# Kernel optimization log

Hardware: AMD Instinct MI355X
Metric: run time of the kernel (lower is better)

The kernel has to match this reference:

```python
import jax, jax.numpy as jnp
import numpy as np

B, N, M, D = 1, 16384, 16384, 3
CHUNK = 2048          # x tile size for the online-min KNN pass
NN_WEIGHT = 1.0       # self.nn_weight
# both_ways=False, free_weight=0, ch_normals_K=0 -> only cham_x branch is active


def setup_inputs() -> dict:
    key = jax.random.key(0)
    k1, k2, k3 = jax.random.split(key, 3)
    # LiDAR-like point clouds, scaled to a ~20 m scene extent
    pc1 = jax.random.normal(k1, (B, N, D), dtype=jnp.float32) * 10.0
    est_flow = jax.random.normal(k2, (B, N, D), dtype=jnp.float32) * 0.1
    pc2 = jax.random.normal(k3, (B, M, D), dtype=jnp.float32) * 10.0
    return {"pc1": pc1, "est_flow": est_flow, "pc2": pc2}


def _knn1_l1_dists(x, y):
    """Per-point min L1 distance from x [N,3] to y [M,3], tiled over x.

    Equivalent to knn_points(x, y, K=1, norm=1).dists[..., 0] without
    materializing the full [N, M] distance matrix.
    """
    n = x.shape[0]
    x_tiles = x.reshape(n // CHUNK, CHUNK, D)

    def tile_min(xc):  # xc: [CHUNK, 3]
        d = jnp.sum(jnp.abs(xc[:, None, :] - y[None, :, :]), axis=-1)  # [CHUNK, M]
        return jnp.min(d, axis=-1)                                     # [CHUNK]

    return jax.lax.map(tile_min, x_tiles).reshape(n)


def reference(pc1, est_flow, pc2):
    x = pc1 + est_flow                                   # deformed cloud [B,N,3]
    cham_x = jax.vmap(_knn1_l1_dists)(x, pc2)            # [B, N]
    cham_y = jnp.float32(0.0)                            # both_ways=False
    freespace_loss = jnp.zeros_like(cham_x)              # free_weight == 0 branch
    chamf_loss = NN_WEIGHT * (cham_x.mean() + cham_y)    # free_weight * 0 omitted
    return (chamf_loss, freespace_loss)
```

## Files before the change

### kernel.cpp

```cpp
#include <hip/hip_runtime.h>


#define TPB 256
#define YSEG 512
#define NITER (YSEG / 16)

typedef float sf16 __attribute__((ext_vector_type(16)));
typedef float sf8  __attribute__((ext_vector_type(8)));

#define SLOAD24(B16, B8, PTR, O16, O8)                                     \
  asm volatile("s_load_dwordx16 %0, %2, " O16 "\n\t"                       \
               "s_load_dwordx8  %1, %2, " O8                               \
               : "=s"(B16), "=s"(B8) : "s"(PTR));

#define SWAIT(B16, B8)                                                     \
  asm volatile("s_waitcnt lgkmcnt(0)" : "+s"(B16), "+s"(B8));

#define DIST2S(MR, AXv, AYv, AZv, Y0X, Y0Y, Y0Z, Y1X, Y1Y, Y1Z)           \
  {                                                                        \
    float t0, t1, t2, t3, t4;                                              \
    asm("v_sub_f32 %1, %9, %6\n\t"                                         \
        "v_sub_f32 %2, %10, %7\n\t"                                        \
        "v_sub_f32 %3, %11, %8\n\t"                                        \
        "v_sub_f32 %4, %12, %6\n\t"                                        \
        "v_sub_f32 %5, %13, %7\n\t"                                        \
        "v_add_f32 %1, |%1|, |%2|\n\t"                                     \
        "v_sub_f32 %2, %14, %8\n\t"                                        \
        "v_add_f32 %4, |%4|, |%5|\n\t"                                     \
        "v_add_f32 %1, %1, |%3|\n\t"                                       \
        "v_add_f32 %4, %4, |%2|\n\t"                                       \
        "v_min3_f32 %0, %0, %1, %4"                                        \
        : "+v"(MR), "=&v"(t0), "=&v"(t1), "=&v"(t2), "=&v"(t3), "=&v"(t4)  \
        : "v"(AXv), "v"(AYv), "v"(AZv),                                    \
          "s"(Y0X), "s"(Y0Y), "s"(Y0Z), "s"(Y1X), "s"(Y1Y), "s"(Y1Z));    \
  }

#define COMPUTE8(G16, G8)                                                  \
  {                                                                        \
    DIST2S(m0, ax, ay, az, G16[0], G16[1], G16[2], G16[3], G16[4], G16[5]); \
    DIST2S(m0, ax, ay, az, G16[6], G16[7], G16[8], G16[9], G16[10], G16[11]); \
    DIST2S(m0, ax, ay, az, G16[12], G16[13], G16[14], G16[15], G8[0], G8[1]); \
    DIST2S(m0, ax, ay, az, G8[2], G8[3], G8[4], G8[5], G8[6], G8[7]);      \
  }

__global__ __launch_bounds__(TPB, 8) void chamfer_kernel(
    const float* __restrict__ pc1, const float* __restrict__ flow,
    const float* __restrict__ pc2, unsigned* __restrict__ minbits,
    int N, int M) {
    const int t = threadIdx.x;

    const int i  = blockIdx.x * TPB + t;
    const int ic = (i < N) ? i : (N - 1);
    const float ax = pc1[3 * ic]     + flow[3 * ic];
    const float ay = pc1[3 * ic + 1] + flow[3 * ic + 1];
    const float az = pc1[3 * ic + 2] + flow[3 * ic + 2];

    float m0 = 3.0e38f;

    const int ybase = blockIdx.y * YSEG;
    const int yend  = (ybase + YSEG < M) ? (ybase + YSEG) : M;

    if (yend - ybase == YSEG) {
        const float* yp = pc2 + (size_t)3 * (size_t)ybase;
        sf16 A16, B16; sf8 A8, B8;
        SLOAD24(A16, A8, yp, "0", "64");
#pragma unroll 1
        for (int it = 0; it < NITER; ++it) {
            SWAIT(A16, A8);
            SLOAD24(B16, B8, yp, "96", "160");
            COMPUTE8(A16, A8);
            SWAIT(B16, B8);
            if (it + 1 < NITER)
                SLOAD24(A16, A8, yp, "192", "256");
            COMPUTE8(B16, B8);
            yp += 48;
        }
    } else {
        for (int j = ybase; j < yend; ++j) {
            const float yx = pc2[3 * j], yy = pc2[3 * j + 1], yz = pc2[3 * j + 2];
            m0 = fminf(m0, fabsf(ax - yx) + fabsf(ay - yy) + fabsf(az - yz));
        }
    }

    if (i < N) atomicMin(&minbits[i], __float_as_uint(m0));
}

__global__ __launch_bounds__(TPB) void finalize_kernel(
    const unsigned* __restrict__ minbits, float* __restrict__ out,
    int N, int out_size, float invN) {
    const int t = threadIdx.x;
    const int stride = gridDim.x * TPB;
    for (int k = blockIdx.x * TPB + t; 1 + k < out_size; k += stride)
        out[1 + k] = 0.0f;

    if (blockIdx.x == 0) {
        float s = 0.0f;
        const uint4* p4 = (const uint4*)minbits;
        const int n4 = N >> 2;
        for (int k = t; k < n4; k += TPB) {
            uint4 v = p4[k];
            s += __uint_as_float(v.x) + __uint_as_float(v.y) +
                 __uint_as_float(v.z) + __uint_as_float(v.w);
        }
        for (int k = (n4 << 2) + t; k < N; k += TPB)
            s += __uint_as_float(minbits[k]);
#pragma unroll
        for (int off = 32; off > 0; off >>= 1) s += __shfl_down(s, off, 64);
        __shared__ float ls[TPB / 64];
        const int wid = t >> 6, lane = t & 63;
        if (lane == 0) ls[wid] = s;
        __syncthreads();
        if (t == 0) {
            float tot = 0.0f;
            for (int w = 0; w < TPB / 64; ++w) tot += ls[w];
            out[0] = tot * invN;
        }
    }
}

extern "C" void kernel_launch(void* const* d_in, const int* in_sizes, int n_in,
                              void* d_out, int out_size, void* d_ws, size_t ws_size,
                              hipStream_t stream) {
    const float* pc1  = (const float*)d_in[0];
    const float* flow = (const float*)d_in[1];
    const float* pc2  = (const float*)d_in[2];
    float* out = (float*)d_out;

    const int N = in_sizes[0] / 3;
    const int M = in_sizes[2] / 3;

    unsigned* minbits = (unsigned*)d_ws;

    hipMemsetAsync(minbits, 0x7F, (size_t)N * sizeof(unsigned), stream);

    const int nbN    = (N + TPB - 1) / TPB;
    const int msplit = (M + YSEG - 1) / YSEG;
    const int nbF    = (out_size - 1 + TPB - 1) / TPB;

    chamfer_kernel<<<dim3(nbN, msplit), TPB, 0, stream>>>(pc1, flow, pc2, minbits, N, M);
    finalize_kernel<<<nbF, TPB, 0, stream>>>(minbits, out, N, out_size, 1.0f / (float)N);
}
```

Before: 43.97 us.

## Replace brute-force KNN with x-slab binning plus bounded window search

Swaps the all-pairs L1 nearest-neighbour scan for a spatial scheme. Both clouds are bucketed into slabs along x with a histogram, a scan and a scatter. A first pass takes an upper bound for each 64-query group from nearby points, and a second pass searches only the x-window that bound allows before atomic-min and a final reduction. This cuts most distance evaluations but adds several small kernel launches and atomics. It also hardcodes the slab range and width (LOX=-64, 1024 slabs of 1/8), which only buckets well for data of this scene scale.

Result: slower. 73.58 us (+67.3%).

```diff
diff --git a/kernel.cpp b/kernel.cpp
--- a/kernel.cpp
+++ b/kernel.cpp
@@ -1,12 +1,24 @@
 #include <hip/hip_runtime.h>
 
 
-#define TPB 256
-#define YSEG 512
-#define NITER (YSEG / 16)
+#define NB   1024
+#define LOX  (-64.0f)
+#define INVW 8.0f
+#define NPAD 16
 
 typedef float sf16 __attribute__((ext_vector_type(16)));
 typedef float sf8  __attribute__((ext_vector_type(8)));
+
+__device__ __forceinline__ int rfl(int v) {
+    return __builtin_amdgcn_readfirstlane(v);
+}
+__device__ __forceinline__ const float* upf(const float* p) {
+    union { const float* p; unsigned u[2]; } a;
+    a.p = p;
+    a.u[0] = (unsigned)__builtin_amdgcn_readfirstlane((int)a.u[0]);
+    a.u[1] = (unsigned)__builtin_amdgcn_readfirstlane((int)a.u[1]);
+    return a.p;
+}
 
 #define SLOAD24(B16, B8, PTR, O16, O8)                                     \
   asm volatile("s_load_dwordx16 %0, %2, " O16 "\n\t"                       \
@@ -35,86 +47,196 @@
           "s"(Y0X), "s"(Y0Y), "s"(Y0Z), "s"(Y1X), "s"(Y1Y), "s"(Y1Z));    \
   }
 
-#define COMPUTE8(G16, G8)                                                  \
+#define COMPUTE8_1(G16, G8)                                                \
   {                                                                        \
-    DIST2S(m0, ax, ay, az, G16[0], G16[1], G16[2], G16[3], G16[4], G16[5]); \
-    DIST2S(m0, ax, ay, az, G16[6], G16[7], G16[8], G16[9], G16[10], G16[11]); \
-    DIST2S(m0, ax, ay, az, G16[12], G16[13], G16[14], G16[15], G8[0], G8[1]); \
-    DIST2S(m0, ax, ay, az, G8[2], G8[3], G8[4], G8[5], G8[6], G8[7]);      \
+    DIST2S(m, qx, qy, qz, G16[0], G16[1], G16[2], G16[3], G16[4], G16[5]); \
+    DIST2S(m, qx, qy, qz, G16[6], G16[7], G16[8], G16[9], G16[10], G16[11]);\
+    DIST2S(m, qx, qy, qz, G16[12], G16[13], G16[14], G16[15], G8[0], G8[1]);\
+    DIST2S(m, qx, qy, qz, G8[2], G8[3], G8[4], G8[5], G8[6], G8[7]);       \
   }
 
-__global__ __launch_bounds__(TPB, 8) void chamfer_kernel(
+__device__ __forceinline__ int slab_of(float x) {
+    int b = (int)((x - LOX) * INVW);
+    return (b < 0) ? 0 : ((b > NB - 1) ? NB - 1 : b);
+}
+
+__global__ __launch_bounds__(256) void hist_kernel(
     const float* __restrict__ pc1, const float* __restrict__ flow,
-    const float* __restrict__ pc2, unsigned* __restrict__ minbits,
-    int N, int M) {
+    const float* __restrict__ pc2, int* __restrict__ hist2,
+    int* __restrict__ histq, int N, int M) {
+    const int i = blockIdx.x * 256 + threadIdx.x;
+    const int stride = gridDim.x * 256;
+    for (int j = i; j < M; j += stride)
+        atomicAdd(&hist2[slab_of(pc2[3 * j])], 1);
+    for (int j = i; j < N; j += stride)
+        atomicAdd(&histq[slab_of(pc1[3 * j] + flow[3 * j])], 1);
+}
+
+__global__ __launch_bounds__(NB) void scan_kernel(
+    const int* __restrict__ hist2, const int* __restrict__ histq,
+    int* __restrict__ base2, int* __restrict__ cursor2, int* __restrict__ cursorq) {
+    __shared__ int sc[NB];
     const int t = threadIdx.x;
-
-    const int i  = blockIdx.x * TPB + t;
-    const int ic = (i < N) ? i : (N - 1);
-    const float ax = pc1[3 * ic]     + flow[3 * ic];
-    const float ay = pc1[3 * ic + 1] + flow[3 * ic + 1];
-    const float az = pc1[3 * ic + 2] + flow[3 * ic + 2];
-
-    float m0 = 3.0e38f;
-
-    const int ybase = blockIdx.y * YSEG;
-    const int yend  = (ybase + YSEG < M) ? (ybase + YSEG) : M;
-
-    if (yend - ybase == YSEG) {
-        const float* yp = pc2 + (size_t)3 * (size_t)ybase;
+    const int* h = (blockIdx.x == 0) ? hist2 : histq;
+    const int hv = h[t];
+    sc[t] = hv;
+    __syncthreads();
+    for (int off = 1; off < NB; off <<= 1) {
+        int v = (t >= off) ? sc[t - off] : 0;
+        __syncthreads();
+        sc[t] += v;
+        __syncthreads();
+    }
+    const int ex = sc[t] - hv;
+    if (blockIdx.x == 0) {
+        base2[t] = ex; cursor2[t] = ex;
+        if (t == NB - 1) base2[NB] = sc[t];
+    } else {
+        cursorq[t] = ex;
+    }
+}
+
+__global__ __launch_bounds__(256) void scatter_kernel(
+    const float* __restrict__ pc1, const float* __restrict__ flow,
+    const float* __restrict__ pc2, int* __restrict__ cursor2,
+    int* __restrict__ cursorq, float* __restrict__ pts2,
+    float4* __restrict__ qs, int N, int M) {
+    const int i = blockIdx.x * 256 + threadIdx.x;
+    const int stride = gridDim.x * 256;
+    for (int j = i; j < M; j += stride) {
+        const float x = pc2[3 * j], y = pc2[3 * j + 1], z = pc2[3 * j + 2];
+        const int pos = atomicAdd(&cursor2[slab_of(x)], 1);
+        pts2[3 * pos] = x; pts2[3 * pos + 1] = y; pts2[3 * pos + 2] = z;
+    }
+    for (int j = i; j < N; j += stride) {
+        const float x = pc1[3 * j] + flow[3 * j];
+        const float y = pc1[3 * j + 1] + flow[3 * j + 1];
+        const float z = pc1[3 * j + 2] + flow[3 * j + 2];
+        const int pos = atomicAdd(&cursorq[slab_of(x)], 1);
+        qs[pos] = make_float4(x, y, z, __int_as_float(j));
+    }
+    if (blockIdx.x == 0 && threadIdx.x < 3 * NPAD)
+        pts2[3 * M + threadIdx.x] = 1.0e30f;
+}
+
+__global__ __launch_bounds__(256) void bound_kernel(
+    const float4* __restrict__ qs, const float* __restrict__ pts2,
+    const int* __restrict__ base2, float* __restrict__ mmaxArr,
+    float* __restrict__ qmin, int N, int M) {
+    const int t = threadIdx.x, w = t >> 6, l = t & 63, g = blockIdx.x;
+    int qi = g * 64 + l; if (qi >= N) qi = N - 1;
+    const float4 qf = qs[qi];
+    const float qx = qf.x, qy = qf.y, qz = qf.z;
+
+    const float qxm = __shfl(qx, 32, 64);
+    const int c = base2[slab_of(qxm)];
+    int ys = c - 224; ys = (ys < 0) ? 0 : ((ys > M - 512) ? M - 512 : ys);
+    ys = rfl(ys);
+
+    float m = 3.0e38f;
+    {
+        const float* yp = upf(pts2 + 3 * (ys + w * 128));
         sf16 A16, B16; sf8 A8, B8;
         SLOAD24(A16, A8, yp, "0", "64");
 #pragma unroll 1
-        for (int it = 0; it < NITER; ++it) {
+        for (int it = 0; it < 8; ++it) {
             SWAIT(A16, A8);
             SLOAD24(B16, B8, yp, "96", "160");
-            COMPUTE8(A16, A8);
+            COMPUTE8_1(A16, A8);
             SWAIT(B16, B8);
-            if (it + 1 < NITER)
-                SLOAD24(A16, A8, yp, "192", "256");
-            COMPUTE8(B16, B8);
+            if (it + 1 < 8) SLOAD24(A16, A8, yp, "192", "256");
+            COMPUTE8_1(B16, B8);
             yp += 48;
         }
-    } else {
-        for (int j = ybase; j < yend; ++j) {
-            const float yx = pc2[3 * j], yy = pc2[3 * j + 1], yz = pc2[3 * j + 2];
-            m0 = fminf(m0, fabsf(ax - yx) + fabsf(ay - yy) + fabsf(az - yz));
+    }
+    __shared__ float smem[4][64];
+    smem[w][l] = m;
+    __syncthreads();
+    if (t < 64) {
+        float m4 = fminf(fminf(smem[0][t], smem[1][t]),
+                         fminf(smem[2][t], smem[3][t]));
+        qmin[__float_as_int(qf.w)] = m4;
+        float mm = m4;
+#pragma unroll
+        for (int off = 1; off < 64; off <<= 1)
+            mm = fmaxf(mm, __shfl_xor(mm, off, 64));
+        if (t == 0) mmaxArr[g] = mm;
+    }
+}
+
+__global__ __launch_bounds__(256) void window_kernel(
+    const float4* __restrict__ qs, const float* __restrict__ pts2,
+    const int* __restrict__ base2, const float* __restrict__ mmaxArr,
+    unsigned* __restrict__ qmin, int N, int M) {
+    const int t = threadIdx.x, w = t >> 6, l = t & 63;
+    const int g = blockIdx.x >> 2, s = blockIdx.x & 3;
+    int qi = g * 64 + l; if (qi >= N) qi = N - 1;
+    const float4 qf = qs[qi];
+    const float qx = qf.x, qy = qf.y, qz = qf.z;
+
+    const float qx0 = __shfl(qx, 0, 64), qx1 = __shfl(qx, 63, 64);
+    const float mm = mmaxArr[g];
+    int bl = (int)((qx0 - mm - LOX) * INVW) - 1;
+    bl = (bl < 0) ? 0 : ((bl > NB - 1) ? NB - 1 : bl);
+    int br = (int)((qx1 + mm - LOX) * INVW) + 1;
+    br = (br < 0) ? 0 : ((br > NB - 1) ? NB - 1 : br);
+    const int B = base2[bl], E = base2[br + 1];
+    const int len = E - B;
+    const int k = s * 4 + w;
+    const int j0 = rfl(B + ((len * k) >> 4));
+    const int j1 = rfl(B + ((len * (k + 1)) >> 4));
+    const int n = j1 - j0;
+
+    float m = 3.0e38f;
+    if (n > 0) {
+        const int NIT = ((((n + 7) >> 3) + 1) & ~1) >> 1;
+        const float* yp = upf(pts2 + 3 * j0);
+        sf16 A16, B16; sf8 A8, B8;
+        SLOAD24(A16, A8, yp, "0", "64");
+#pragma unroll 1
+        for (int it = 0; it < NIT; ++it) {
+            SWAIT(A16, A8);
+            SLOAD24(B16, B8, yp, "96", "160");
+            COMPUTE8_1(A16, A8);
+            SWAIT(B16, B8);
+            if (it + 1 < NIT) SLOAD24(A16, A8, yp, "192", "256");
+            COMPUTE8_1(B16, B8);
+            yp += 48;
         }
     }
-
-    if (i < N) atomicMin(&minbits[i], __float_as_uint(m0));
-}
-
-__global__ __launch_bounds__(TPB) void finalize_kernel(
-    const unsigned* __restrict__ minbits, float* __restrict__ out,
+    __shared__ float smem[4][64];
+    smem[w][l] = m;
+    __syncthreads();
+    if (t < 64) {
+        const float m4 = fminf(fminf(smem[0][t], smem[1][t]),
+                               fminf(smem[2][t], smem[3][t]));
+        atomicMin(&qmin[__float_as_int(qf.w)], __float_as_uint(m4));
+    }
+}
+
+__global__ __launch_bounds__(1024) void final_kernel(
+    const unsigned* __restrict__ qmin, float* __restrict__ out,
     int N, int out_size, float invN) {
     const int t = threadIdx.x;
-    const int stride = gridDim.x * TPB;
-    for (int k = blockIdx.x * TPB + t; 1 + k < out_size; k += stride)
-        out[1 + k] = 0.0f;
-
-    if (blockIdx.x == 0) {
-        float s = 0.0f;
-        const uint4* p4 = (const uint4*)minbits;
-        const int n4 = N >> 2;
-        for (int k = t; k < n4; k += TPB) {
-            uint4 v = p4[k];
-            s += __uint_as_float(v.x) + __uint_as_float(v.y) +
-                 __uint_as_float(v.z) + __uint_as_float(v.w);
-        }
-        for (int k = (n4 << 2) + t; k < N; k += TPB)
-            s += __uint_as_float(minbits[k]);
+    for (int kk = t; 1 + kk < out_size; kk += 1024) out[1 + kk] = 0.0f;
+    float sacc = 0.0f;
+    const uint4* p4 = (const uint4*)qmin;
+    for (int kk = t; kk < N / 4; kk += 1024) {
+        const uint4 v = p4[kk];
+        sacc += __uint_as_float(v.x) + __uint_as_float(v.y) +
+                __uint_as_float(v.z) + __uint_as_float(v.w);
+    }
+    for (int kk = (N / 4) * 4 + t; kk < N; kk += 1024)
+        sacc += __uint_as_float(qmin[kk]);
 #pragma unroll
-        for (int off = 32; off > 0; off >>= 1) s += __shfl_down(s, off, 64);
-        __shared__ float ls[TPB / 64];
-        const int wid = t >> 6, lane = t & 63;
-        if (lane == 0) ls[wid] = s;
-        __syncthreads();
-        if (t == 0) {
-            float tot = 0.0f;
-            for (int w = 0; w < TPB / 64; ++w) tot += ls[w];
-            out[0] = tot * invN;
-        }
+    for (int off = 32; off; off >>= 1) sacc += __shfl_down(sacc, off, 64);
+    __shared__ float ls[16];
+    if ((t & 63) == 0) ls[t >> 6] = sacc;
+    __syncthreads();
+    if (t == 0) {
+        float tot = 0.0f;
+        for (int w2 = 0; w2 < 16; ++w2) tot += ls[w2];
+        out[0] = tot * invN;
     }
 }
 
@@ -129,14 +251,27 @@
     const int N = in_sizes[0] / 3;
     const int M = in_sizes[2] / 3;
 
-    unsigned* minbits = (unsigned*)d_ws;
-
-    hipMemsetAsync(minbits, 0x7F, (size_t)N * sizeof(unsigned), stream);
-
-    const int nbN    = (N + TPB - 1) / TPB;
-    const int msplit = (M + YSEG - 1) / YSEG;
-    const int nbF    = (out_size - 1 + TPB - 1) / TPB;
-
-    chamfer_kernel<<<dim3(nbN, msplit), TPB, 0, stream>>>(pc1, flow, pc2, minbits, N, M);
-    finalize_kernel<<<nbF, TPB, 0, stream>>>(minbits, out, N, out_size, 1.0f / (float)N);
-}
+    char* ws = (char*)d_ws;
+    int*    hist2   = (int*)(ws + 0);
+    int*    histq   = (int*)(ws + 4096);
+    int*    base2   = (int*)(ws + 8192);
+    int*    cursor2 = (int*)(ws + 16384);
+    int*    cursorq = (int*)(ws + 20480);
+    float*  mmaxArr = (float*)(ws + 24576);
+    float*  qmin    = (float*)(ws + 28672);
+    float*  pts2    = (float*)(ws + 94208);
+    float4* qs      = (float4*)(ws + 291328);
+
+    const int NG = (N + 63) / 64;
+
+    hipMemsetAsync(hist2, 0, 2 * NB * sizeof(int), stream);
+    hist_kernel<<<64, 256, 0, stream>>>(pc1, flow, pc2, hist2, histq, N, M);
+    scan_kernel<<<2, NB, 0, stream>>>(hist2, histq, base2, cursor2, cursorq);
+    scatter_kernel<<<64, 256, 0, stream>>>(pc1, flow, pc2, cursor2, cursorq,
+                                           pts2, qs, N, M);
+    bound_kernel<<<NG, 256, 0, stream>>>(qs, pts2, base2, mmaxArr, qmin, N, M);
+    window_kernel<<<NG * 4, 256, 0, stream>>>(qs, pts2, base2, mmaxArr,
+                                              (unsigned*)qmin, N, M);
+    final_kernel<<<1, 1024, 0, stream>>>((const unsigned*)qmin, out, N,
+                                         out_size, 1.0f / (float)N);
+}
```
